# Performance work log

Hardware: AMD Instinct MI355X
Metric: run time of the kernel (lower is better)

The kernel has to match this reference:

```python
import jax, jax.numpy as jnp
import numpy as np
from jax import lax

X, H, L, VT, ET = 4096, 1024, 8, 512, 1024


def setup_inputs() -> dict:
    key = jax.random.key(0)
    ks = jax.random.split(key, 10)
    stdv = 1.0 / np.sqrt(H)
    u = lambda k, shape, s: jax.random.uniform(k, shape, jnp.float32, -s, s)
    inp = {
        "input_x": jax.random.normal(ks[0], (X,), jnp.float32),
        "h_prev": jax.random.normal(ks[1], (L, H), jnp.float32),
        # fused gate weights: order [input, forget, output, state] along the 4H axis
        "Wg": u(ks[2], (L, 4 * H, X + 2 * H), stdv),
        # combined bias = Linear bias + extra b_* parameter (same math, one tensor)
        "bg": u(ks[3], (L, 4 * H), 2.0 * stdv),
        "old_state": u(ks[4], (L, H), stdv),
        "Wy": u(ks[5], (VT, L * H), 1.0 / np.sqrt(L * H)),
        "by": u(ks[6], (VT,), 1.0 / np.sqrt(L * H)),
        "We": u(ks[7], (ET, L * H), 1.0 / np.sqrt(L * H)),
        "be": u(ks[8], (ET,), 1.0 / np.sqrt(L * H)),
    }
    return inp


def reference(input_x, h_prev, Wg, bg, old_state, Wy, by, We, be):
    def step(prev_layer, per_layer):
        W, b, c_old, h_t = per_layer
        # semicolon_input = [input_x ; previous_time ; previous_layer]
        z = jnp.concatenate([input_x, h_t, prev_layer])  # (X+2H,)
        gates = W @ z + b                                 # (4H,) fused 4 GEMVs
        i_g, f_g, o_g, s_g = jnp.split(gates, 4)
        new_state = jax.nn.sigmoid(f_g) * c_old + jax.nn.sigmoid(i_g) * jnp.tanh(s_g)
        new_hidden = jax.nn.sigmoid(o_g) * jnp.tanh(new_state)
        return new_hidden, new_hidden

    init = jnp.zeros((H,), input_x.dtype)  # hidden_previous_layer starts at 0
    _, hidden = lax.scan(step, init, (Wg, bg, old_state, h_prev))  # (L, H)
    flat = hidden.reshape(L * H)
    output = Wy @ flat + by
    interface = We @ flat + be
    return output, interface
```

## Files before the change

### kernel.cpp

```cpp
#include <hip/hip_runtime.h>
#include <hip/hip_bf16.h>
#include <cstddef>


#define XDIM 4096
#define HDIM 1024
#define LNUM 8
#define ZDIM 6144
#define ZPAR 5120
#define VT 512
#define ET 1024

__device__ __forceinline__ float sigmoidf_(float v) {
    return 1.0f / (1.0f + expf(-v));
}

__global__ __launch_bounds__(256, 4) void prefix_kernel(
    const float* __restrict__ x,
    const float* __restrict__ hprev,
    const float* __restrict__ Wg,
    const float* __restrict__ bg,
    const float* __restrict__ old_state,
    float* __restrict__ partial,
    float* __restrict__ hidden)
{
    __shared__ float z[ZPAR];
    __shared__ float g2[4][2];

    const int tid  = threadIdx.x;
    const int wave = tid >> 6;
    const int lane = tid & 63;
    const int l    = blockIdx.x >> 9;
    const int h0   = (blockIdx.x & 511) * 2;

    for (int i = tid; i < XDIM / 4; i += 256)
        reinterpret_cast<float4*>(z)[i] = reinterpret_cast<const float4*>(x)[i];
    reinterpret_cast<float4*>(z + XDIM)[tid] =
        reinterpret_cast<const float4*>(hprev + (size_t)l * HDIM)[tid];
    __syncthreads();

    const size_t rA = (size_t)l * 4096 + (size_t)wave * HDIM + h0;
    const size_t rB = rA + 1;
    const float4* __restrict__ WA = reinterpret_cast<const float4*>(Wg + rA * ZDIM);
    const float4* __restrict__ WB = reinterpret_cast<const float4*>(Wg + rB * ZDIM);
    const float4* __restrict__ z4 = reinterpret_cast<const float4*>(z);

    float accA = 0.0f, accB = 0.0f;
    #pragma unroll 4
    for (int p = 0; p < 20; ++p) {
        const int idx = p * 64 + lane;
        float4 wa = WA[idx];
        float4 wb = WB[idx];
        float4 v  = z4[idx];
        accA += wa.x * v.x + wa.y * v.y + wa.z * v.z + wa.w * v.w;
        accB += wb.x * v.x + wb.y * v.y + wb.z * v.z + wb.w * v.w;
    }
    #pragma unroll
    for (int off = 32; off > 0; off >>= 1) {
        accA += __shfl_down(accA, off, 64);
        accB += __shfl_down(accB, off, 64);
    }

    if (l > 0) {
        if (lane == 0) {
            partial[rA] = accA + bg[rA];
            partial[rB] = accB + bg[rB];
        }
    } else {
        if (lane == 0) {
            g2[wave][0] = accA + bg[rA];
            g2[wave][1] = accB + bg[rB];
        }
        __syncthreads();
        if (tid == 0) {
            #pragma unroll
            for (int k = 0; k < 2; ++k) {
                const float ig = sigmoidf_(g2[0][k]);
                const float fg = sigmoidf_(g2[1][k]);
                const float og = sigmoidf_(g2[2][k]);
                const float sg = tanhf(g2[3][k]);
                const float ns = fg * old_state[h0 + k] + ig * sg;
                hidden[h0 + k] = og * tanhf(ns);
            }
        }
    }
}

__global__ __launch_bounds__(256) void carry_kernel(
    const float* __restrict__ Wg,
    const float* __restrict__ partial,
    const float* __restrict__ old_state,
    const float* __restrict__ hidden_prev,
    float* __restrict__ hidden_out,
    int l)
{
    __shared__ float hp[HDIM];
    __shared__ float gred[4];

    const int tid  = threadIdx.x;
    const int wave = tid >> 6;
    const int lane = tid & 63;
    const int h    = blockIdx.x;

    reinterpret_cast<float4*>(hp)[tid] =
        reinterpret_cast<const float4*>(hidden_prev)[tid];
    __syncthreads();

    const size_t row = (size_t)l * 4096 + (size_t)wave * HDIM + h;
    const float4* __restrict__ W4 =
        reinterpret_cast<const float4*>(Wg + row * ZDIM + ZPAR);
    const float4* __restrict__ h4 = reinterpret_cast<const float4*>(hp);

    float acc = 0.0f;
    #pragma unroll
    for (int p = 0; p < 4; ++p) {
        const int idx = p * 64 + lane;
        float4 w = W4[idx];
        float4 v = h4[idx];
        acc += w.x * v.x + w.y * v.y + w.z * v.z + w.w * v.w;
    }
    #pragma unroll
    for (int off = 32; off > 0; off >>= 1)
        acc += __shfl_down(acc, off, 64);
    if (lane == 0)
        gred[wave] = acc + partial[row];
    __syncthreads();

    if (tid == 0) {
        const float ig = sigmoidf_(gred[0]);
        const float fg = sigmoidf_(gred[1]);
        const float og = sigmoidf_(gred[2]);
        const float sg = tanhf(gred[3]);
        const float ns = fg * old_state[(size_t)l * HDIM + h] + ig * sg;
        hidden_out[h] = og * tanhf(ns);
    }
}

__global__ __launch_bounds__(256) void head_kernel(
    const float* __restrict__ Wy, const float* __restrict__ by,
    const float* __restrict__ We, const float* __restrict__ be,
    const float* __restrict__ flat,
    float* __restrict__ out)
{
    __shared__ float gred[4];

    const int tid  = threadIdx.x;
    const int wave = tid >> 6;
    const int lane = tid & 63;
    const int r    = blockIdx.x;

    const float* __restrict__ W;
    float b;
    if (r < VT) { W = Wy + (size_t)r * (LNUM * HDIM);        b = by[r]; }
    else        { W = We + (size_t)(r - VT) * (LNUM * HDIM); b = be[r - VT]; }

    const float4* __restrict__ W4 = reinterpret_cast<const float4*>(W);
    const float4* __restrict__ f4 = reinterpret_cast<const float4*>(flat);

    float acc = 0.0f;
    #pragma unroll
    for (int j = 0; j < 8; ++j) {
        const int idx = wave * 512 + j * 64 + lane;
        float4 w = W4[idx];
        float4 v = f4[idx];
        acc += w.x * v.x + w.y * v.y + w.z * v.z + w.w * v.w;
    }
    #pragma unroll
    for (int off = 32; off > 0; off >>= 1)
        acc += __shfl_down(acc, off, 64);
    if (lane == 0) gred[wave] = acc;
    __syncthreads();

    if (tid == 0)
        out[r] = gred[0] + gred[1] + gred[2] + gred[3] + b;
}

extern "C" void kernel_launch(void* const* d_in, const int* in_sizes, int n_in,
                              void* d_out, int out_size, void* d_ws, size_t ws_size,
                              hipStream_t stream)
{
    const float* x         = (const float*)d_in[0];
    const float* hprev     = (const float*)d_in[1];
    const float* Wg        = (const float*)d_in[2];
    const float* bg        = (const float*)d_in[3];
    const float* old_state = (const float*)d_in[4];
    const float* Wy        = (const float*)d_in[5];
    const float* by        = (const float*)d_in[6];
    const float* We        = (const float*)d_in[7];
    const float* be        = (const float*)d_in[8];
    float* out = (float*)d_out;

    float* hidden  = (float*)d_ws;
    float* partial = hidden + LNUM * HDIM;

    prefix_kernel<<<4096, 256, 0, stream>>>(
        x, hprev, Wg, bg, old_state, partial, hidden);

    for (int l = 1; l < LNUM; ++l) {
        carry_kernel<<<1024, 256, 0, stream>>>(
            Wg, partial, old_state,
            hidden + (size_t)(l - 1) * HDIM,
            hidden + (size_t)l * HDIM, l);
    }

    head_kernel<<<VT + ET, 256, 0, stream>>>(Wy, by, We, be, hidden, out);
}
```

Before: 170.5 us.

## Fuse per-layer carry launches into persistent kernel with atomic layer barriers

Result: slower. 633.9 us (+271.9%).

```diff
diff --git a/kernel.cpp b/kernel.cpp
--- a/kernel.cpp
+++ b/kernel.cpp
@@ -10,6 +10,8 @@
 #define ZPAR 5120
 #define VT 512
 #define ET 1024
+#define NCNT 16
+#define GRP (1024 / NCNT)
 
 __device__ __forceinline__ float sigmoidf_(float v) {
     return 1.0f / (1.0f + expf(-v));
@@ -22,7 +24,8 @@
     const float* __restrict__ bg,
     const float* __restrict__ old_state,
     float* __restrict__ partial,
-    float* __restrict__ hidden)
+    float* __restrict__ hidden,
+    int* __restrict__ cnt)
 {
     __shared__ float z[ZPAR];
     __shared__ float g2[4][2];
@@ -32,6 +35,9 @@
     const int lane = tid & 63;
     const int l    = blockIdx.x >> 9;
     const int h0   = (blockIdx.x & 511) * 2;
+
+    if (blockIdx.x == 0 && tid < LNUM * NCNT)
+        cnt[tid] = 0;
 
     for (int i = tid; i < XDIM / 4; i += 256)
         reinterpret_cast<float4*>(z)[i] = reinterpret_cast<const float4*>(x)[i];
@@ -86,13 +92,12 @@
     }
 }
 
-__global__ __launch_bounds__(256) void carry_kernel(
+__global__ __launch_bounds__(256, 4) void carry_chain_kernel(
     const float* __restrict__ Wg,
     const float* __restrict__ partial,
     const float* __restrict__ old_state,
-    const float* __restrict__ hidden_prev,
-    float* __restrict__ hidden_out,
-    int l)
+    float* __restrict__ hidden,
+    int* __restrict__ cnt)
 {
     __shared__ float hp[HDIM];
     __shared__ float gred[4];
@@ -102,37 +107,66 @@
     const int lane = tid & 63;
     const int h    = blockIdx.x;
 
-    reinterpret_cast<float4*>(hp)[tid] =
-        reinterpret_cast<const float4*>(hidden_prev)[tid];
-    __syncthreads();
-
-    const size_t row = (size_t)l * 4096 + (size_t)wave * HDIM + h;
+    size_t row = (size_t)4096 + (size_t)wave * HDIM + h;
+    {
+        const float4* __restrict__ W4 =
+            reinterpret_cast<const float4*>(Wg + row * ZDIM + ZPAR);
+        asm volatile("" ::: "memory");
+    }
     const float4* __restrict__ W4 =
         reinterpret_cast<const float4*>(Wg + row * ZDIM + ZPAR);
-    const float4* __restrict__ h4 = reinterpret_cast<const float4*>(hp);
-
-    float acc = 0.0f;
-    #pragma unroll
-    for (int p = 0; p < 4; ++p) {
-        const int idx = p * 64 + lane;
-        float4 w = W4[idx];
-        float4 v = h4[idx];
-        acc += w.x * v.x + w.y * v.y + w.z * v.z + w.w * v.w;
-    }
-    #pragma unroll
-    for (int off = 32; off > 0; off >>= 1)
-        acc += __shfl_down(acc, off, 64);
-    if (lane == 0)
-        gred[wave] = acc + partial[row];
-    __syncthreads();
-
-    if (tid == 0) {
-        const float ig = sigmoidf_(gred[0]);
-        const float fg = sigmoidf_(gred[1]);
-        const float og = sigmoidf_(gred[2]);
-        const float sg = tanhf(gred[3]);
-        const float ns = fg * old_state[(size_t)l * HDIM + h] + ig * sg;
-        hidden_out[h] = og * tanhf(ns);
+    float4 w0 = W4[lane], w1 = W4[64 + lane], w2 = W4[128 + lane], w3 = W4[192 + lane];
+    float part = partial[row];
+
+    for (int l = 1; l < LNUM; ++l) {
+        if (l > 1) {
+            if (tid < NCNT) {
+                while (__hip_atomic_load(&cnt[(l - 1) * NCNT + tid],
+                                         __ATOMIC_ACQUIRE,
+                                         __HIP_MEMORY_SCOPE_AGENT) < GRP)
+                    __builtin_amdgcn_s_sleep(2);
+            }
+        }
+        __syncthreads();
+
+        reinterpret_cast<float4*>(hp)[tid] =
+            reinterpret_cast<const float4*>(hidden + (size_t)(l - 1) * HDIM)[tid];
+        __syncthreads();
+
+        const float4* __restrict__ h4 = reinterpret_cast<const float4*>(hp);
+        float4 v0 = h4[lane], v1 = h4[64 + lane], v2 = h4[128 + lane], v3 = h4[192 + lane];
+        float acc = w0.x * v0.x + w0.y * v0.y + w0.z * v0.z + w0.w * v0.w
+                  + w1.x * v1.x + w1.y * v1.y + w1.z * v1.z + w1.w * v1.w
+                  + w2.x * v2.x + w2.y * v2.y + w2.z * v2.z + w2.w * v2.w
+                  + w3.x * v3.x + w3.y * v3.y + w3.z * v3.z + w3.w * v3.w;
+
+        float part_next = 0.0f;
+        if (l + 1 < LNUM) {
+            row += 4096;
+            const float4* __restrict__ NW4 =
+                reinterpret_cast<const float4*>(Wg + row * ZDIM + ZPAR);
+            w0 = NW4[lane]; w1 = NW4[64 + lane]; w2 = NW4[128 + lane]; w3 = NW4[192 + lane];
+            part_next = partial[row];
+        }
+
+        #pragma unroll
+        for (int off = 32; off > 0; off >>= 1)
+            acc += __shfl_down(acc, off, 64);
+        if (lane == 0)
+            gred[wave] = acc + part;
+        __syncthreads();
+
+        if (tid == 0) {
+            const float ig = sigmoidf_(gred[0]);
+            const float fg = sigmoidf_(gred[1]);
+            const float og = sigmoidf_(gred[2]);
+            const float sg = tanhf(gred[3]);
+            const float ns = fg * old_state[(size_t)l * HDIM + h] + ig * sg;
+            hidden[(size_t)l * HDIM + h] = og * tanhf(ns);
+            __hip_atomic_fetch_add(&cnt[l * NCNT + (h & (NCNT - 1))], 1,
+                                   __ATOMIC_RELEASE, __HIP_MEMORY_SCOPE_AGENT);
+        }
+        part = part_next;
     }
 }
 
@@ -192,16 +226,13 @@
 
     float* hidden  = (float*)d_ws;
     float* partial = hidden + LNUM * HDIM;
+    int*   cnt     = (int*)(partial + LNUM * 4 * HDIM);
 
     prefix_kernel<<<4096, 256, 0, stream>>>(
-        x, hprev, Wg, bg, old_state, partial, hidden);
-
-    for (int l = 1; l < LNUM; ++l) {
-        carry_kernel<<<1024, 256, 0, stream>>>(
-            Wg, partial, old_state,
-            hidden + (size_t)(l - 1) * HDIM,
-            hidden + (size_t)l * HDIM, l);
-    }
+        x, hprev, Wg, bg, old_state, partial, hidden, cnt);
+
+    carry_chain_kernel<<<1024, 256, 0, stream>>>(
+        Wg, partial, old_state, hidden, cnt);
 
     head_kernel<<<VT + ET, 256, 0, stream>>>(Wy, by, We, be, hidden, out);
 }
```

## Drop layer-parallel prefix GEMV and compute each layer fully per step

Applied to the files above, without the earlier changes.

New measurement: 172.3 us. Within noise of the previous version (+1.1%).

```diff
diff --git a/kernel.cpp b/kernel.cpp
--- a/kernel.cpp
+++ b/kernel.cpp
@@ -15,115 +15,54 @@
     return 1.0f / (1.0f + expf(-v));
 }
 
-__global__ __launch_bounds__(256, 4) void prefix_kernel(
+__global__ __launch_bounds__(256, 4) void layer_kernel(
     const float* __restrict__ x,
     const float* __restrict__ hprev,
     const float* __restrict__ Wg,
     const float* __restrict__ bg,
     const float* __restrict__ old_state,
-    float* __restrict__ partial,
-    float* __restrict__ hidden)
-{
-    __shared__ float z[ZPAR];
-    __shared__ float g2[4][2];
+    const float* __restrict__ hidden_prev,
+    float* __restrict__ hidden_out,
+    int l)
+{
+    __shared__ float z[ZDIM];
+    __shared__ float gred[4];
 
     const int tid  = threadIdx.x;
     const int wave = tid >> 6;
     const int lane = tid & 63;
-    const int l    = blockIdx.x >> 9;
-    const int h0   = (blockIdx.x & 511) * 2;
+    const int h    = blockIdx.x;
 
     for (int i = tid; i < XDIM / 4; i += 256)
         reinterpret_cast<float4*>(z)[i] = reinterpret_cast<const float4*>(x)[i];
     reinterpret_cast<float4*>(z + XDIM)[tid] =
         reinterpret_cast<const float4*>(hprev + (size_t)l * HDIM)[tid];
-    __syncthreads();
-
-    const size_t rA = (size_t)l * 4096 + (size_t)wave * HDIM + h0;
-    const size_t rB = rA + 1;
-    const float4* __restrict__ WA = reinterpret_cast<const float4*>(Wg + rA * ZDIM);
-    const float4* __restrict__ WB = reinterpret_cast<const float4*>(Wg + rB * ZDIM);
+    reinterpret_cast<float4*>(z + ZPAR)[tid] =
+        reinterpret_cast<const float4*>(hidden_prev)[tid];
+    __syncthreads();
+
+    const size_t row = (size_t)l * 4096 + (size_t)wave * HDIM + h;
+    const float4* __restrict__ W4 = reinterpret_cast<const float4*>(Wg + row * ZDIM);
     const float4* __restrict__ z4 = reinterpret_cast<const float4*>(z);
 
     float accA = 0.0f, accB = 0.0f;
     #pragma unroll 4
-    for (int p = 0; p < 20; ++p) {
-        const int idx = p * 64 + lane;
-        float4 wa = WA[idx];
-        float4 wb = WB[idx];
-        float4 v  = z4[idx];
-        accA += wa.x * v.x + wa.y * v.y + wa.z * v.z + wa.w * v.w;
-        accB += wb.x * v.x + wb.y * v.y + wb.z * v.z + wb.w * v.w;
-    }
-    #pragma unroll
-    for (int off = 32; off > 0; off >>= 1) {
-        accA += __shfl_down(accA, off, 64);
-        accB += __shfl_down(accB, off, 64);
-    }
-
-    if (l > 0) {
-        if (lane == 0) {
-            partial[rA] = accA + bg[rA];
-            partial[rB] = accB + bg[rB];
-        }
-    } else {
-        if (lane == 0) {
-            g2[wave][0] = accA + bg[rA];
-            g2[wave][1] = accB + bg[rB];
-        }
-        __syncthreads();
-        if (tid == 0) {
-            #pragma unroll
-            for (int k = 0; k < 2; ++k) {
-                const float ig = sigmoidf_(g2[0][k]);
-                const float fg = sigmoidf_(g2[1][k]);
-                const float og = sigmoidf_(g2[2][k]);
-                const float sg = tanhf(g2[3][k]);
-                const float ns = fg * old_state[h0 + k] + ig * sg;
-                hidden[h0 + k] = og * tanhf(ns);
-            }
-        }
-    }
-}
-
-__global__ __launch_bounds__(256) void carry_kernel(
-    const float* __restrict__ Wg,
-    const float* __restrict__ partial,
-    const float* __restrict__ old_state,
-    const float* __restrict__ hidden_prev,
-    float* __restrict__ hidden_out,
-    int l)
-{
-    __shared__ float hp[HDIM];
-    __shared__ float gred[4];
-
-    const int tid  = threadIdx.x;
-    const int wave = tid >> 6;
-    const int lane = tid & 63;
-    const int h    = blockIdx.x;
-
-    reinterpret_cast<float4*>(hp)[tid] =
-        reinterpret_cast<const float4*>(hidden_prev)[tid];
-    __syncthreads();
-
-    const size_t row = (size_t)l * 4096 + (size_t)wave * HDIM + h;
-    const float4* __restrict__ W4 =
-        reinterpret_cast<const float4*>(Wg + row * ZDIM + ZPAR);
-    const float4* __restrict__ h4 = reinterpret_cast<const float4*>(hp);
-
-    float acc = 0.0f;
-    #pragma unroll
-    for (int p = 0; p < 4; ++p) {
-        const int idx = p * 64 + lane;
-        float4 w = W4[idx];
-        float4 v = h4[idx];
-        acc += w.x * v.x + w.y * v.y + w.z * v.z + w.w * v.w;
-    }
+    for (int p = 0; p < 12; ++p) {
+        const int ia = p * 64 + lane;
+        const int ib = ia + 768;
+        float4 wa = W4[ia];
+        float4 wb = W4[ib];
+        float4 va = z4[ia];
+        float4 vb = z4[ib];
+        accA += wa.x * va.x + wa.y * va.y + wa.z * va.z + wa.w * va.w;
+        accB += wb.x * vb.x + wb.y * vb.y + wb.z * vb.z + wb.w * vb.w;
+    }
+    float acc = accA + accB;
     #pragma unroll
     for (int off = 32; off > 0; off >>= 1)
         acc += __shfl_down(acc, off, 64);
     if (lane == 0)
-        gred[wave] = acc + partial[row];
+        gred[wave] = acc + bg[row];
     __syncthreads();
 
     if (tid == 0) {
@@ -132,6 +71,62 @@
         const float og = sigmoidf_(gred[2]);
         const float sg = tanhf(gred[3]);
         const float ns = fg * old_state[(size_t)l * HDIM + h] + ig * sg;
+        hidden_out[h] = og * tanhf(ns);
+    }
+}
+
+__global__ __launch_bounds__(256, 4) void layer0_kernel(
+    const float* __restrict__ x,
+    const float* __restrict__ hprev,
+    const float* __restrict__ Wg,
+    const float* __restrict__ bg,
+    const float* __restrict__ old_state,
+    float* __restrict__ hidden_out)
+{
+    __shared__ float z[ZPAR];
+    __shared__ float gred[4];
+
+    const int tid  = threadIdx.x;
+    const int wave = tid >> 6;
+    const int lane = tid & 63;
+    const int h    = blockIdx.x;
+
+    for (int i = tid; i < XDIM / 4; i += 256)
+        reinterpret_cast<float4*>(z)[i] = reinterpret_cast<const float4*>(x)[i];
+    reinterpret_cast<float4*>(z + XDIM)[tid] =
+        reinterpret_cast<const float4*>(hprev)[tid];
+    __syncthreads();
+
+    const size_t row = (size_t)wave * HDIM + h;
+    const float4* __restrict__ W4 = reinterpret_cast<const float4*>(Wg + row * ZDIM);
+    const float4* __restrict__ z4 = reinterpret_cast<const float4*>(z);
+
+    float accA = 0.0f, accB = 0.0f;
+    #pragma unroll 5
+    for (int p = 0; p < 10; ++p) {
+        const int ia = p * 64 + lane;
+        const int ib = ia + 640;
+        float4 wa = W4[ia];
+        float4 wb = W4[ib];
+        float4 va = z4[ia];
+        float4 vb = z4[ib];
+        accA += wa.x * va.x + wa.y * va.y + wa.z * va.z + wa.w * va.w;
+        accB += wb.x * vb.x + wb.y * vb.y + wb.z * vb.z + wb.w * vb.w;
+    }
+    float acc = accA + accB;
+    #pragma unroll
+    for (int off = 32; off > 0; off >>= 1)
+        acc += __shfl_down(acc, off, 64);
+    if (lane == 0)
+        gred[wave] = acc + bg[row];
+    __syncthreads();
+
+    if (tid == 0) {
+        const float ig = sigmoidf_(gred[0]);
+        const float fg = sigmoidf_(gred[1]);
+        const float og = sigmoidf_(gred[2]);
+        const float sg = tanhf(gred[3]);
+        const float ns = fg * old_state[h] + ig * sg;
         hidden_out[h] = og * tanhf(ns);
     }
 }
@@ -190,15 +185,14 @@
     const float* be        = (const float*)d_in[8];
     float* out = (float*)d_out;
 
-    float* hidden  = (float*)d_ws;
-    float* partial = hidden + LNUM * HDIM;
-
-    prefix_kernel<<<4096, 256, 0, stream>>>(
-        x, hprev, Wg, bg, old_state, partial, hidden);
+    float* hidden = (float*)d_ws;
+
+    layer0_kernel<<<1024, 256, 0, stream>>>(
+        x, hprev, Wg, bg, old_state, hidden);
 
     for (int l = 1; l < LNUM; ++l) {
-        carry_kernel<<<1024, 256, 0, stream>>>(
-            Wg, partial, old_state,
+        layer_kernel<<<1024, 256, 0, stream>>>(
+            x, hprev, Wg, bg, old_state,
             hidden + (size_t)(l - 1) * HDIM,
             hidden + (size_t)l * HDIM, l);
     }
```

## Fold output-head GEMV into per-layer carry kernels to overlap with recurrence

Applied to the files above, without the earlier changes.

After: 169.0 us (median of 2 runs). No clear change (-0.8%).

```diff
diff --git a/kernel.cpp b/kernel.cpp
--- a/kernel.cpp
+++ b/kernel.cpp
@@ -10,9 +10,13 @@
 #define ZPAR 5120
 #define VT 512
 #define ET 1024
+#define NR (VT + ET)
 
 __device__ __forceinline__ float sigmoidf_(float v) {
     return 1.0f / (1.0f + expf(-v));
+}
+__device__ __forceinline__ float dot4_(float4 a, float4 b) {
+    return a.x * b.x + a.y * b.y + a.z * b.z + a.w * b.w;
 }
 
 __global__ __launch_bounds__(256, 4) void prefix_kernel(
@@ -52,8 +56,8 @@
         float4 wa = WA[idx];
         float4 wb = WB[idx];
         float4 v  = z4[idx];
-        accA += wa.x * v.x + wa.y * v.y + wa.z * v.z + wa.w * v.w;
-        accB += wb.x * v.x + wb.y * v.y + wb.z * v.z + wb.w * v.w;
+        accA += dot4_(wa, v);
+        accB += dot4_(wb, v);
     }
     #pragma unroll
     for (int off = 32; off > 0; off >>= 1) {
@@ -92,38 +96,61 @@
     const float* __restrict__ old_state,
     const float* __restrict__ hidden_prev,
     float* __restrict__ hidden_out,
+    const float* __restrict__ Wy,
+    const float* __restrict__ We,
+    float* __restrict__ headacc,
     int l)
 {
-    __shared__ float hp[HDIM];
     __shared__ float gred[4];
+    __shared__ float hred[2][4];
 
     const int tid  = threadIdx.x;
     const int wave = tid >> 6;
     const int lane = tid & 63;
     const int h    = blockIdx.x;
-
-    reinterpret_cast<float4*>(hp)[tid] =
-        reinterpret_cast<const float4*>(hidden_prev)[tid];
-    __syncthreads();
+    const bool do_head = (blockIdx.x < NR / 2);
 
     const size_t row = (size_t)l * 4096 + (size_t)wave * HDIM + h;
     const float4* __restrict__ W4 =
         reinterpret_cast<const float4*>(Wg + row * ZDIM + ZPAR);
-    const float4* __restrict__ h4 = reinterpret_cast<const float4*>(hp);
-
-    float acc = 0.0f;
-    #pragma unroll
-    for (int p = 0; p < 4; ++p) {
-        const int idx = p * 64 + lane;
-        float4 w = W4[idx];
-        float4 v = h4[idx];
-        acc += w.x * v.x + w.y * v.y + w.z * v.z + w.w * v.w;
-    }
+    const float4* __restrict__ h4 =
+        reinterpret_cast<const float4*>(hidden_prev);
+
+    float4 w0 = W4[lane], w1 = W4[64 + lane], w2 = W4[128 + lane], w3 = W4[192 + lane];
+    float4 v0 = h4[lane], v1 = h4[64 + lane], v2 = h4[128 + lane], v3 = h4[192 + lane];
+
+    int r0 = 0, r1 = 0;
+    float4 a0, a1;
+    if (do_head) {
+        r0 = 2 * blockIdx.x;
+        r1 = r0 + 1;
+        const float* Wr0 = (r0 < VT) ? (Wy + (size_t)r0 * (LNUM * HDIM))
+                                     : (We + (size_t)(r0 - VT) * (LNUM * HDIM));
+        const float* Wr1 = (r1 < VT) ? (Wy + (size_t)r1 * (LNUM * HDIM))
+                                     : (We + (size_t)(r1 - VT) * (LNUM * HDIM));
+        const int idx = (l - 1) * 256 + wave * 64 + lane;
+        a0 = reinterpret_cast<const float4*>(Wr0)[idx];
+        a1 = reinterpret_cast<const float4*>(Wr1)[idx];
+    }
+
+    float acc = dot4_(w0, v0) + dot4_(w1, v1) + dot4_(w2, v2) + dot4_(w3, v3);
     #pragma unroll
     for (int off = 32; off > 0; off >>= 1)
         acc += __shfl_down(acc, off, 64);
     if (lane == 0)
         gred[wave] = acc + partial[row];
+
+    if (do_head) {
+        float4 hv = (wave == 0) ? v0 : (wave == 1) ? v1 : (wave == 2) ? v2 : v3;
+        float d0 = dot4_(a0, hv);
+        float d1 = dot4_(a1, hv);
+        #pragma unroll
+        for (int off = 32; off > 0; off >>= 1) {
+            d0 += __shfl_down(d0, off, 64);
+            d1 += __shfl_down(d1, off, 64);
+        }
+        if (lane == 0) { hred[0][wave] = d0; hred[1][wave] = d1; }
+    }
     __syncthreads();
 
     if (tid == 0) {
@@ -134,12 +161,23 @@
         const float ns = fg * old_state[(size_t)l * HDIM + h] + ig * sg;
         hidden_out[h] = og * tanhf(ns);
     }
-}
-
-__global__ __launch_bounds__(256) void head_kernel(
+    if (do_head) {
+        if (tid == 64) {
+            const float s = hred[0][0] + hred[0][1] + hred[0][2] + hred[0][3];
+            headacc[r0] = ((l == 1) ? 0.0f : headacc[r0]) + s;
+        }
+        if (tid == 128) {
+            const float s = hred[1][0] + hred[1][1] + hred[1][2] + hred[1][3];
+            headacc[r1] = ((l == 1) ? 0.0f : headacc[r1]) + s;
+        }
+    }
+}
+
+__global__ __launch_bounds__(256) void head_finish_kernel(
     const float* __restrict__ Wy, const float* __restrict__ by,
     const float* __restrict__ We, const float* __restrict__ be,
-    const float* __restrict__ flat,
+    const float* __restrict__ hidden,
+    const float* __restrict__ headacc,
     float* __restrict__ out)
 {
     __shared__ float gred[4];
@@ -149,22 +187,16 @@
     const int lane = tid & 63;
     const int r    = blockIdx.x;
 
-    const float* __restrict__ W;
+    const float* W;
     float b;
     if (r < VT) { W = Wy + (size_t)r * (LNUM * HDIM);        b = by[r]; }
     else        { W = We + (size_t)(r - VT) * (LNUM * HDIM); b = be[r - VT]; }
 
-    const float4* __restrict__ W4 = reinterpret_cast<const float4*>(W);
-    const float4* __restrict__ f4 = reinterpret_cast<const float4*>(flat);
-
-    float acc = 0.0f;
-    #pragma unroll
-    for (int j = 0; j < 8; ++j) {
-        const int idx = wave * 512 + j * 64 + lane;
-        float4 w = W4[idx];
-        float4 v = f4[idx];
-        acc += w.x * v.x + w.y * v.y + w.z * v.z + w.w * v.w;
-    }
+    const int idx = 7 * 256 + wave * 64 + lane;
+    float4 w = reinterpret_cast<const float4*>(W)[idx];
+    float4 v = reinterpret_cast<const float4*>(hidden)[idx];
+
+    float acc = dot4_(w, v);
     #pragma unroll
     for (int off = 32; off > 0; off >>= 1)
         acc += __shfl_down(acc, off, 64);
@@ -172,7 +204,7 @@
     __syncthreads();
 
     if (tid == 0)
-        out[r] = gred[0] + gred[1] + gred[2] + gred[3] + b;
+        out[r] = headacc[r] + gred[0] + gred[1] + gred[2] + gred[3] + b;
 }
 
 extern "C" void kernel_launch(void* const* d_in, const int* in_sizes, int n_in,
@@ -192,6 +224,7 @@
 
     float* hidden  = (float*)d_ws;
     float* partial = hidden + LNUM * HDIM;
+    float* headacc = partial + LNUM * 4 * HDIM;
 
     prefix_kernel<<<4096, 256, 0, stream>>>(
         x, hprev, Wg, bg, old_state, partial, hidden);
@@ -200,8 +233,10 @@
         carry_kernel<<<1024, 256, 0, stream>>>(
             Wg, partial, old_state,
             hidden + (size_t)(l - 1) * HDIM,
-            hidden + (size_t)l * HDIM, l);
-    }
-
-    head_kernel<<<VT + ET, 256, 0, stream>>>(Wy, by, We, be, hidden, out);
-}
+            hidden + (size_t)l * HDIM,
+            Wy, We, headacc, l);
+    }
+
+    head_finish_kernel<<<NR, 256, 0, stream>>>(
+        Wy, by, We, be, hidden, headacc, out);
+}
```
